# Performance work log

Hardware: AMD Instinct MI355X
Metric: run time of the kernel (lower is better)

The kernel has to match this reference:

```python
import jax, jax.numpy as jnp
import numpy as np

VOCAB = 128
NUM_PATHS = 100     # num_paths sampled from the lattice
NBEST_SCALE = 0.5   # scale on scores before sampling (k2.random_paths)
TEMPERATURE = 1.0   # logprob temperature before normalization
BLANK = 0           # CTC blank token


def setup_inputs() -> dict:
    key = jax.random.key(0)
    k1, k2, k3, k4 = jax.random.split(key, 4)
    B, T, L = 8, 500, 100
    logits = jax.random.normal(k1, (B, T, VOCAB), jnp.float32)
    emissions = jax.nn.log_softmax(logits, -1)  # acoustic-model log-probs (N, T, C)
    emissions_lengths = jax.random.randint(k2, (B,), 400, T + 1).astype(jnp.int32)
    labels = jax.random.randint(k3, (B, L), 1, VOCAB).astype(jnp.int32)
    labels_length = jax.random.randint(k4, (B,), 80, L + 1).astype(jnp.int32)
    return {"emissions": emissions, "emissions_lengths": emissions_lengths,
            "labels": labels, "labels_length": labels_length}


def _mwer(emissions, emissions_lengths, labels, labels_length):
    B, T, V = emissions.shape
    L = labels.shape[1]
    P = NUM_PATHS
    key = jax.random.key(1)
    # --- N-best path sampling: Gumbel perturbation of nbest_scale-scaled log-probs ---
    u = jax.random.uniform(key, (B, P, T, V), emissions.dtype, 1e-6, 1.0 - 1e-6)
    g = -jnp.log(-jnp.log(u))
    tokens = jnp.argmax(emissions[:, None] * NBEST_SCALE + g, axis=-1)  # (B, P, T)
    frame_mask = jnp.arange(T)[None, None, :] < emissions_lengths[:, None, None]
    # path log-prob under the model (unscaled scores), temperature-scaled
    lp = jnp.take_along_axis(emissions[:, None], tokens[..., None], axis=-1)[..., 0]
    path_logp = jnp.sum(jnp.where(frame_mask, lp, 0.0), axis=-1) / TEMPERATURE  # (B, P)
    # --- CTC collapse (ctc_topo semantics: drop blanks + repeats) into padded hyps ---
    prev = jnp.concatenate([jnp.full_like(tokens[..., :1], -1), tokens[..., :-1]], -1)
    keep = (tokens != BLANK) & (tokens != prev) & frame_mask
    pos = jnp.where(keep, jnp.cumsum(keep, -1) - 1, T)  # dropped frames -> dump slot T
    BP = B * P
    tok2, pos2 = tokens.reshape(BP, T), pos.reshape(BP, T)
    hyp = jnp.full((BP, T + 1), -1, tokens.dtype).at[jnp.arange(BP)[:, None], pos2].set(tok2)[:, :T]
    hyp_len = keep.reshape(BP, T).sum(-1)
    # --- Levenshtein alignment: exact edit distance hyp vs ref (vectorized DP) ---
    refs = jnp.repeat(labels, P, axis=0)             # (BP, L)  hyp_to_ref_map
    ref_len = jnp.repeat(labels_length, P, axis=0)   # (BP,)
    dp0 = jnp.broadcast_to(jnp.arange(L + 1, dtype=jnp.int32), (BP, L + 1))
    js = jnp.arange(L + 1, dtype=jnp.int32)[None, :]

    def step(dp, x):
        h, valid = x  # hyp token (BP,), valid flag (BP,)
        cost = (refs != h[:, None]).astype(jnp.int32)                       # (BP, L)
        cand = jnp.concatenate([dp[:, :1] + 1,
                                jnp.minimum(dp[:, 1:] + 1, dp[:, :-1] + cost)], 1)
        # insertion chain new[j] = min(cand[j], new[j-1]+1) via min-plus prefix
        new = jax.lax.cummin(cand - js, axis=1) + js
        return jnp.where(valid[:, None], new, dp), None

    valid = jnp.arange(T)[:, None] < hyp_len[None, :]  # (T, BP)
    dp, _ = jax.lax.scan(step, dp0, (hyp.T, valid))
    wers = jnp.take_along_axis(dp, ref_len[:, None], 1)[:, 0].reshape(B, P)
    wers = jax.lax.stop_gradient(wers.astype(emissions.dtype))
    # --- MWER: normalize path posteriors per utterance, expected WER, 'mean' ---
    prob = jax.nn.softmax(path_logp, axis=1)
    return jnp.mean(prob * wers)


def reference(emissions, emissions_lengths, labels, labels_length):
    return _mwer(emissions, emissions_lengths, labels, labels_length)
```

## Files before the change

kernel.cpp:

```cpp
#include <hip/hip_runtime.h>
#include <stdint.h>

#define NB 8
#define NP 100
#define NT 500
#define NV 128
#define NBP 800
#define TILE 8
#define TROWS 5

typedef unsigned long long u64;

#define ROTL(x, r) __builtin_amdgcn_alignbit((x), (x), 32 - (r))

__device__ __forceinline__ uint32_t threefry01_lo(uint32_t x0, uint32_t x1) {
  const uint32_t k0 = 0u, k1 = 1u;
  const uint32_t k2 = 0x1BD11BDAu ^ k0 ^ k1;
  x0 += k0; x1 += k1;
#define TF_R(r) { x0 += x1; x1 = ROTL(x1, r); x1 ^= x0; }
  TF_R(13) TF_R(15) TF_R(26) TF_R(6)
  x0 += k1; x1 += k2 + 1u;
  TF_R(17) TF_R(29) TF_R(16) TF_R(24)
  x0 += k2; x1 += k0 + 2u;
  TF_R(13) TF_R(15) TF_R(26) TF_R(6)
  x0 += k0; x1 += k1 + 3u;
  TF_R(17) TF_R(29) TF_R(16) TF_R(24)
  x0 += k1; x1 += k2 + 4u;
  TF_R(13) TF_R(15) TF_R(26) TF_R(6)
  x1 += k0 + 5u;
#undef TF_R
  return x1;
}

__global__ __launch_bounds__(512) void k_sample(
    const float* __restrict__ em, const int* __restrict__ elen,
    int2* __restrict__ tl) {
  const int b = blockIdx.x;
  const int t0 = blockIdx.y * TROWS;
  __shared__ float se[TROWS][NV];
  __shared__ float snw[TROWS][NV];
  const int tid = threadIdx.x;
  const int el = elen[b];
  for (int i = tid; i < TROWS * NV; i += 512) {
    const int r = i >> 7, v = i & 127;
    const float e = em[(size_t)((b * NT + t0 + r) << 7) + v];
    se[r][v] = e;
    snw[r][v] = -__builtin_amdgcn_exp2f(e * -0.7213475204444817f);
  }
  __syncthreads();
  if (tid >= TROWS * NP) return;
  const int r = tid / NP, p = tid - r * NP;
  const int t = t0 + r;
  if (t >= el) return;
  const uint32_t base = (uint32_t)((b * NP + p) * NT + t) << 7;
  const float span = (float)(1.0 - 1e-6) - 1e-6f;
  float best = 3.0e38f;
  int bi = 0;
#pragma unroll
  for (int v = 0; v < NV; v++) {
    const uint32_t rnd = threefry01_lo(0u, base + (uint32_t)v);
    const float f = __uint_as_float((rnd >> 9) | 0x3f800000u) - 1.0f;
    const float u = fmaxf(1e-6f, fmaf(f, span, 1e-6f));
    const float sc = __log2f(u) * snw[r][v];
    if (sc < best) { best = sc; bi = v; }
  }
  tl[t * NBP + b * NP + p] = make_int2(bi, __float_as_int(se[r][bi]));
}

struct DpState {
  u64 Pv0, Pv1, Mv0, Mv1;
  int score, prev;
  double logp;
};

struct TileData {
  int cc[TILE];
  float ll[TILE];
  u64 eq0[TILE], eq1[TILE];
};

__device__ __forceinline__ void load_tile(int2 (&buf)[TILE], int tile,
                                          const int2* __restrict__ tl, int bpc) {
#pragma unroll
  for (int i = 0; i < TILE; i++) {
    int t = tile * TILE + i;
    t = t < NT ? t : NT - 1;
    buf[i] = tl[t * NBP + bpc];
  }
}

__device__ __forceinline__ void extract(const int2 (&buf)[TILE],
                                        const uint32_t (*pq)[NV], TileData& td) {
#pragma unroll
  for (int i = 0; i < TILE; i++) {
    td.cc[i] = buf[i].x;
    td.ll[i] = __int_as_float(buf[i].y);
    const int c = buf[i].x & 127;
    td.eq0[i] = (u64)pq[0][c] | ((u64)pq[1][c] << 32);
    td.eq1[i] = (u64)pq[2][c] | ((u64)pq[3][c] << 32);
  }
}

__device__ __forceinline__ void process_tile(const TileData& td, int tile,
                                             int myel, int hw, u64 hmask,
                                             DpState& st) {
#pragma unroll
  for (int i = 0; i < TILE; i++) {
    const int t = tile * TILE + i;
    if (t >= myel) break;
    const int c = td.cc[i];
    const bool kept = (c != 0) && (c != st.prev);
    st.logp += (double)td.ll[i];
    st.prev = c;
    if (kept) {
      const u64 Eq0 = td.eq0[i], Eq1 = td.eq1[i];
      const u64 Xv0 = Eq0 | st.Mv0, Xv1 = Eq1 | st.Mv1;
      const u64 EP0 = Eq0 & st.Pv0, EP1 = Eq1 & st.Pv1;
      const u64 sA = EP0 + st.Pv0;
      const u64 sB = EP1 + st.Pv1 + (sA < EP0 ? 1ull : 0ull);
      const u64 Xh0 = (sA ^ st.Pv0) | Eq0;
      const u64 Xh1 = (sB ^ st.Pv1) | Eq1;
      const u64 Ph0 = st.Mv0 | ~(Xh0 | st.Pv0);
      const u64 Ph1 = st.Mv1 | ~(Xh1 | st.Pv1);
      const u64 Mh0 = st.Pv0 & Xh0, Mh1 = st.Pv1 & Xh1;
      st.score += (int)(((hw ? Ph1 : Ph0) & hmask) != 0);
      st.score -= (int)(((hw ? Mh1 : Mh0) & hmask) != 0);
      const u64 nPh1 = (Ph1 << 1) | (Ph0 >> 63);
      const u64 nPh0 = (Ph0 << 1) | 1ull;
      const u64 nMh1 = (Mh1 << 1) | (Mh0 >> 63);
      const u64 nMh0 = (Mh0 << 1);
      st.Pv0 = nMh0 | ~(Xv0 | nPh0);
      st.Pv1 = nMh1 | ~(Xv1 | nPh1);
      st.Mv0 = nPh0 & Xv0;
      st.Mv1 = nPh1 & Xv1;
    }
  }
}

__global__ __launch_bounds__(128) void k_dp(
    const int2* __restrict__ tl,
    const int* __restrict__ elen, const int* __restrict__ labels,
    const int* __restrict__ llen,
    float* __restrict__ wer, float* __restrict__ logp_out) {
  __shared__ uint32_t pq[4][NV];
  const int b = blockIdx.x;
  const int tid = threadIdx.x;
  const int m = llen[b];
  {
    const int c = tid;
    const int* __restrict__ lab = labels + b * 100;
    uint32_t a0 = 0, a1 = 0, a2 = 0, a3 = 0;
    const int e0 = m < 32 ? m : 32, e1 = m < 64 ? m : 64;
    const int e2 = m < 96 ? m : 96, e3 = m;
    for (int i = 0; i < e0; i++)  a0 |= (uint32_t)(lab[i] == c) << i;
    for (int i = 32; i < e1; i++) a1 |= (uint32_t)(lab[i] == c) << (i - 32);
    for (int i = 64; i < e2; i++) a2 |= (uint32_t)(lab[i] == c) << (i - 64);
    for (int i = 96; i < e3; i++) a3 |= (uint32_t)(lab[i] == c) << (i - 96);
    pq[0][c] = a0; pq[1][c] = a1; pq[2][c] = a2; pq[3][c] = a3;
  }
  __syncthreads();
  const bool active = (tid < NP);
  const int bpc = b * NP + (active ? tid : NP - 1);
  const int myel = elen[b];
  const int ntiles = (myel + TILE - 1) / TILE;

  DpState st;
  st.Pv0 = ~0ull; st.Pv1 = ~0ull; st.Mv0 = 0ull; st.Mv1 = 0ull;
  st.score = m; st.prev = -1; st.logp = 0.0;
  const int hw = (m - 1) >> 6;
  const u64 hmask = 1ull << ((m - 1) & 63);

  int2 bufA[TILE], bufB[TILE];
  TileData TA, TB;
  load_tile(bufA, 0, tl, bpc);
  load_tile(bufB, 1, tl, bpc);
  extract(bufA, pq, TA);
  for (int tile = 0; tile < ntiles; tile += 2) {
    if (tile + 2 < ntiles) load_tile(bufA, tile + 2, tl, bpc);
    extract(bufB, pq, TB);
    process_tile(TA, tile, myel, hw, hmask, st);
    if (tile + 3 < ntiles) load_tile(bufB, tile + 3, tl, bpc);
    if (tile + 2 < ntiles) extract(bufA, pq, TA);
    if (tile + 1 < ntiles) process_tile(TB, tile + 1, myel, hw, hmask, st);
  }
  if (active) { wer[bpc] = (float)st.score; logp_out[bpc] = (float)st.logp; }
}

__global__ __launch_bounds__(512) void k_final(
    const float* __restrict__ wer, const float* __restrict__ logp,
    float* __restrict__ out) {
  __shared__ float partial[NB];
  const int w = threadIdx.x >> 6, lane = threadIdx.x & 63;
  const int base = w * NP;
  float l0 = (lane < NP) ? logp[base + lane] : -1e30f;
  float l1 = (lane + 64 < NP) ? logp[base + lane + 64] : -1e30f;
  float mx = fmaxf(l0, l1);
  for (int off = 1; off < 64; off <<= 1) mx = fmaxf(mx, __shfl_xor(mx, off));
  const float e0 = (lane < NP) ? __expf(l0 - mx) : 0.0f;
  const float e1 = (lane + 64 < NP) ? __expf(l1 - mx) : 0.0f;
  const float w0 = (lane < NP) ? wer[base + lane] : 0.0f;
  const float w1 = (lane + 64 < NP) ? wer[base + lane + 64] : 0.0f;
  float s = e0 + e1;
  float a = e0 * w0 + e1 * w1;
  for (int off = 1; off < 64; off <<= 1) {
    s += __shfl_xor(s, off);
    a += __shfl_xor(a, off);
  }
  if (lane == 0) partial[w] = a / s;
  __syncthreads();
  if (threadIdx.x == 0) {
    float tot = 0.0f;
    for (int i = 0; i < NB; i++) tot += partial[i];
    out[0] = tot * (1.0f / (float)NBP);
  }
}

extern "C" void kernel_launch(void* const* d_in, const int* in_sizes, int n_in,
                              void* d_out, int out_size, void* d_ws, size_t ws_size,
                              hipStream_t stream) {
  const float* em     = (const float*)d_in[0];
  const int*   elen   = (const int*)d_in[1];
  const int*   labels = (const int*)d_in[2];
  const int*   llen   = (const int*)d_in[3];
  float* out = (float*)d_out;
  char* ws = (char*)d_ws;
  int2*  tlb  = (int2*)ws;
  float* wer  = (float*)(ws + (size_t)NT * NBP * 8);
  float* logp = (float*)(ws + (size_t)NT * NBP * 8 + NBP * 4);

  k_sample<<<dim3(NB, NT / TROWS), dim3(512), 0, stream>>>(em, elen, tlb);
  k_dp<<<dim3(NB), dim3(128), 0, stream>>>(tlb, elen, labels, llen, wer, logp);
  k_final<<<dim3(1), dim3(512), 0, stream>>>(wer, logp, out);
}
```

Measured before the change: 226.7 us.

## Compute two paths per thread in sampling and DP kernels with 64-thread blocks

The sampling kernel now uses a flat grid of 64-thread blocks, each thread computing two paths. The two paths share the same emission weights, and their independent threefry chains can interleave for more ILP. The DP kernel shrinks to one 64-thread wave per utterance, with each lane advancing two independent bit-parallel Levenshtein states. The tile size is halved to hold down register pressure. This cuts idle lanes and adds instruction-level parallelism, at the cost of more registers per thread and lower occupancy in the sampling kernel.

```diff
diff --git a/kernel.cpp b/kernel.cpp
--- a/kernel.cpp
+++ b/kernel.cpp
@@ -6,8 +6,7 @@
 #define NT 500
 #define NV 128
 #define NBP 800
-#define TILE 8
-#define TROWS 5
+#define TILE 4
 
 typedef unsigned long long u64;
 
@@ -32,39 +31,51 @@
   return x1;
 }
 
-__global__ __launch_bounds__(512) void k_sample(
+__global__ __launch_bounds__(64) void k_sample(
     const float* __restrict__ em, const int* __restrict__ elen,
     int2* __restrict__ tl) {
-  const int b = blockIdx.x;
-  const int t0 = blockIdx.y * TROWS;
-  __shared__ float se[TROWS][NV];
-  __shared__ float snw[TROWS][NV];
+  __shared__ float se[3][NV + 1];
+  __shared__ float snw[3][NV + 1];
   const int tid = threadIdx.x;
-  const int el = elen[b];
-  for (int i = tid; i < TROWS * NV; i += 512) {
+  const int g0 = blockIdx.x * 64;
+  const int R0 = g0 / 50;
+  for (int i = tid; i < 3 * NV; i += 64) {
     const int r = i >> 7, v = i & 127;
-    const float e = em[(size_t)((b * NT + t0 + r) << 7) + v];
+    int R = R0 + r; R = R < NB * NT ? R : NB * NT - 1;
+    const float e = em[(size_t)R * NV + v];
     se[r][v] = e;
     snw[r][v] = -__builtin_amdgcn_exp2f(e * -0.7213475204444817f);
   }
   __syncthreads();
-  if (tid >= TROWS * NP) return;
-  const int r = tid / NP, p = tid - r * NP;
-  const int t = t0 + r;
-  if (t >= el) return;
-  const uint32_t base = (uint32_t)((b * NP + p) * NT + t) << 7;
+  const int g = g0 + tid;
+  const int R = g / 50;
+  const int pp = g - R * 50;
+  const int b = R / NT;
+  const int t = R - b * NT;
+  if (t >= elen[b]) return;
+  const int r = R - R0;
+  const uint32_t base0 = (uint32_t)((b * NP + 2 * pp) * NT + t) << 7;
+  const uint32_t base1 = base0 + (uint32_t)(NT << 7);
   const float span = (float)(1.0 - 1e-6) - 1e-6f;
-  float best = 3.0e38f;
-  int bi = 0;
-#pragma unroll
+  float best0 = 3.0e38f, best1 = 3.0e38f;
+  int bi0 = 0, bi1 = 0;
+#pragma unroll 8
   for (int v = 0; v < NV; v++) {
-    const uint32_t rnd = threefry01_lo(0u, base + (uint32_t)v);
-    const float f = __uint_as_float((rnd >> 9) | 0x3f800000u) - 1.0f;
-    const float u = fmaxf(1e-6f, fmaf(f, span, 1e-6f));
-    const float sc = __log2f(u) * snw[r][v];
-    if (sc < best) { best = sc; bi = v; }
-  }
-  tl[t * NBP + b * NP + p] = make_int2(bi, __float_as_int(se[r][bi]));
+    const uint32_t r0 = threefry01_lo(0u, base0 + (uint32_t)v);
+    const uint32_t r1 = threefry01_lo(0u, base1 + (uint32_t)v);
+    const float f0 = __uint_as_float((r0 >> 9) | 0x3f800000u) - 1.0f;
+    const float f1 = __uint_as_float((r1 >> 9) | 0x3f800000u) - 1.0f;
+    const float u0 = fmaxf(1e-6f, fmaf(f0, span, 1e-6f));
+    const float u1 = fmaxf(1e-6f, fmaf(f1, span, 1e-6f));
+    const float w = snw[r][v];
+    const float s0 = __log2f(u0) * w;
+    const float s1 = __log2f(u1) * w;
+    if (s0 < best0) { best0 = s0; bi0 = v; }
+    if (s1 < best1) { best1 = s1; bi1 = v; }
+  }
+  const int ob = t * NBP + b * NP + 2 * pp;
+  tl[ob]     = make_int2(bi0, __float_as_int(se[r][bi0]));
+  tl[ob + 1] = make_int2(bi1, __float_as_int(se[r][bi1]));
 }
 
 struct DpState {
@@ -73,14 +84,14 @@
   double logp;
 };
 
-struct TileData {
+struct Ext {
   int cc[TILE];
   float ll[TILE];
   u64 eq0[TILE], eq1[TILE];
 };
 
-__device__ __forceinline__ void load_tile(int2 (&buf)[TILE], int tile,
-                                          const int2* __restrict__ tl, int bpc) {
+__device__ __forceinline__ void load4(int2 (&buf)[TILE], int tile,
+                                      const int2* __restrict__ tl, int bpc) {
 #pragma unroll
   for (int i = 0; i < TILE; i++) {
     int t = tile * TILE + i;
@@ -89,31 +100,30 @@
   }
 }
 
-__device__ __forceinline__ void extract(const int2 (&buf)[TILE],
-                                        const uint32_t (*pq)[NV], TileData& td) {
+__device__ __forceinline__ void extract4(const int2 (&buf)[TILE],
+                                         const uint32_t (*pq)[NV], Ext& e) {
 #pragma unroll
   for (int i = 0; i < TILE; i++) {
-    td.cc[i] = buf[i].x;
-    td.ll[i] = __int_as_float(buf[i].y);
+    e.cc[i] = buf[i].x;
+    e.ll[i] = __int_as_float(buf[i].y);
     const int c = buf[i].x & 127;
-    td.eq0[i] = (u64)pq[0][c] | ((u64)pq[1][c] << 32);
-    td.eq1[i] = (u64)pq[2][c] | ((u64)pq[3][c] << 32);
-  }
-}
-
-__device__ __forceinline__ void process_tile(const TileData& td, int tile,
-                                             int myel, int hw, u64 hmask,
-                                             DpState& st) {
+    e.eq0[i] = (u64)pq[0][c] | ((u64)pq[1][c] << 32);
+    e.eq1[i] = (u64)pq[2][c] | ((u64)pq[3][c] << 32);
+  }
+}
+
+__device__ __forceinline__ void proc4(const Ext& e, int tile, int myel,
+                                      int hw, u64 hmask, DpState& st) {
 #pragma unroll
   for (int i = 0; i < TILE; i++) {
     const int t = tile * TILE + i;
     if (t >= myel) break;
-    const int c = td.cc[i];
+    const int c = e.cc[i];
     const bool kept = (c != 0) && (c != st.prev);
-    st.logp += (double)td.ll[i];
+    st.logp += (double)e.ll[i];
     st.prev = c;
     if (kept) {
-      const u64 Eq0 = td.eq0[i], Eq1 = td.eq1[i];
+      const u64 Eq0 = e.eq0[i], Eq1 = e.eq1[i];
       const u64 Xv0 = Eq0 | st.Mv0, Xv1 = Eq1 | st.Mv1;
       const u64 EP0 = Eq0 & st.Pv0, EP1 = Eq1 & st.Pv1;
       const u64 sA = EP0 + st.Pv0;
@@ -137,7 +147,7 @@
   }
 }
 
-__global__ __launch_bounds__(128) void k_dp(
+__global__ __launch_bounds__(64) void k_dp(
     const int2* __restrict__ tl,
     const int* __restrict__ elen, const int* __restrict__ labels,
     const int* __restrict__ llen,
@@ -147,43 +157,56 @@
   const int tid = threadIdx.x;
   const int m = llen[b];
   {
-    const int c = tid;
     const int* __restrict__ lab = labels + b * 100;
-    uint32_t a0 = 0, a1 = 0, a2 = 0, a3 = 0;
     const int e0 = m < 32 ? m : 32, e1 = m < 64 ? m : 64;
     const int e2 = m < 96 ? m : 96, e3 = m;
-    for (int i = 0; i < e0; i++)  a0 |= (uint32_t)(lab[i] == c) << i;
-    for (int i = 32; i < e1; i++) a1 |= (uint32_t)(lab[i] == c) << (i - 32);
-    for (int i = 64; i < e2; i++) a2 |= (uint32_t)(lab[i] == c) << (i - 64);
-    for (int i = 96; i < e3; i++) a3 |= (uint32_t)(lab[i] == c) << (i - 96);
-    pq[0][c] = a0; pq[1][c] = a1; pq[2][c] = a2; pq[3][c] = a3;
+#pragma unroll
+    for (int h = 0; h < 2; h++) {
+      const int c = tid + h * 64;
+      uint32_t a0 = 0, a1 = 0, a2 = 0, a3 = 0;
+      for (int i = 0; i < e0; i++)  a0 |= (uint32_t)(lab[i] == c) << i;
+      for (int i = 32; i < e1; i++) a1 |= (uint32_t)(lab[i] == c) << (i - 32);
+      for (int i = 64; i < e2; i++) a2 |= (uint32_t)(lab[i] == c) << (i - 64);
+      for (int i = 96; i < e3; i++) a3 |= (uint32_t)(lab[i] == c) << (i - 96);
+      pq[0][c] = a0; pq[1][c] = a1; pq[2][c] = a2; pq[3][c] = a3;
+    }
   }
   __syncthreads();
-  const bool active = (tid < NP);
-  const int bpc = b * NP + (active ? tid : NP - 1);
+  const bool active = (tid < 50);
+  const int lane = active ? tid : 49;
+  const int pa = b * NP + lane;
+  const int pb = pa + 50;
   const int myel = elen[b];
   const int ntiles = (myel + TILE - 1) / TILE;
 
-  DpState st;
-  st.Pv0 = ~0ull; st.Pv1 = ~0ull; st.Mv0 = 0ull; st.Mv1 = 0ull;
-  st.score = m; st.prev = -1; st.logp = 0.0;
+  DpState sA, sB;
+  sA.Pv0 = ~0ull; sA.Pv1 = ~0ull; sA.Mv0 = 0ull; sA.Mv1 = 0ull;
+  sA.score = m; sA.prev = -1; sA.logp = 0.0;
+  sB = sA;
   const int hw = (m - 1) >> 6;
   const u64 hmask = 1ull << ((m - 1) & 63);
 
-  int2 bufA[TILE], bufB[TILE];
-  TileData TA, TB;
-  load_tile(bufA, 0, tl, bpc);
-  load_tile(bufB, 1, tl, bpc);
-  extract(bufA, pq, TA);
+  int2 a0[TILE], b0[TILE], a1[TILE], b1[TILE];
+  Ext eAa, eAb, eBa, eBb;
+  load4(a0, 0, tl, pa); load4(b0, 0, tl, pb);
+  load4(a1, 1, tl, pa); load4(b1, 1, tl, pb);
+  extract4(a0, pq, eAa); extract4(b0, pq, eAb);
   for (int tile = 0; tile < ntiles; tile += 2) {
-    if (tile + 2 < ntiles) load_tile(bufA, tile + 2, tl, bpc);
-    extract(bufB, pq, TB);
-    process_tile(TA, tile, myel, hw, hmask, st);
-    if (tile + 3 < ntiles) load_tile(bufB, tile + 3, tl, bpc);
-    if (tile + 2 < ntiles) extract(bufA, pq, TA);
-    if (tile + 1 < ntiles) process_tile(TB, tile + 1, myel, hw, hmask, st);
-  }
-  if (active) { wer[bpc] = (float)st.score; logp_out[bpc] = (float)st.logp; }
+    if (tile + 2 < ntiles) { load4(a0, tile + 2, tl, pa); load4(b0, tile + 2, tl, pb); }
+    extract4(a1, pq, eBa); extract4(b1, pq, eBb);
+    proc4(eAa, tile, myel, hw, hmask, sA);
+    proc4(eAb, tile, myel, hw, hmask, sB);
+    if (tile + 3 < ntiles) { load4(a1, tile + 3, tl, pa); load4(b1, tile + 3, tl, pb); }
+    if (tile + 2 < ntiles) { extract4(a0, pq, eAa); extract4(b0, pq, eAb); }
+    if (tile + 1 < ntiles) {
+      proc4(eBa, tile + 1, myel, hw, hmask, sA);
+      proc4(eBb, tile + 1, myel, hw, hmask, sB);
+    }
+  }
+  if (active) {
+    wer[pa] = (float)sA.score; logp_out[pa] = (float)sA.logp;
+    wer[pb] = (float)sB.score; logp_out[pb] = (float)sB.logp;
+  }
 }
 
 __global__ __launch_bounds__(512) void k_final(
@@ -228,7 +251,7 @@
   float* wer  = (float*)(ws + (size_t)NT * NBP * 8);
   float* logp = (float*)(ws + (size_t)NT * NBP * 8 + NBP * 4);
 
-  k_sample<<<dim3(NB, NT / TROWS), dim3(512), 0, stream>>>(em, elen, tlb);
-  k_dp<<<dim3(NB), dim3(128), 0, stream>>>(tlb, elen, labels, llen, wer, logp);
+  k_sample<<<dim3(NB * NT * 50 / 64), dim3(64), 0, stream>>>(em, elen, tlb);
+  k_dp<<<dim3(NB), dim3(64), 0, stream>>>(tlb, elen, labels, llen, wer, logp);
   k_final<<<dim3(1), dim3(512), 0, stream>>>(wer, logp, out);
 }
```

Measured after the change: 325.6 us. 1.44x slower.
